# Kernel tuning notes

Hardware: AMD Instinct MI355X
Metric: run time of the kernel (lower is better)

Reference implementation:

```python
import jax, jax.numpy as jnp
import numpy as np

SITE, DIM = 8, 16
B = 8192
D = 2 * DIM

# --- static Z2-graded (Grassmann) bookkeeping -------------------------------
# Each edge (d, d) has parity 0 for the first d indices, parity 1 for the rest.
# Merging two graded edges reorders the flat product index so that all
# even-parity combinations come first (stable/lex within each sector).

def _merge_order(pA, pB):
    p = (pA[:, None] ^ pB[None, :]).reshape(-1)
    return np.argsort(p, kind='stable')

_P1 = np.array([0, 1])                                        # edge (1,1)
_PD = np.concatenate([np.zeros(DIM, np.int64), np.ones(DIM, np.int64)])  # edge (d,d)
ORDER_DD = _merge_order(_PD, _PD); INV_DD = np.argsort(ORDER_DD)
ORDER_1D = _merge_order(_P1, _PD); INV_1D = np.argsort(ORDER_1D)
ORDER_11 = _merge_order(_P1, _P1)                             # = [0,3,1,2]
MASK_X = jnp.asarray((_P1[:, None] ^ _PD[None, :]) == 0, jnp.float32)   # (2, D)
MASK_G2 = jnp.asarray((_PD[:, None] ^ _PD[None, :]) == 0, jnp.float32)  # (D, D)
MASK_G3 = jnp.asarray((_PD[:, None, None] ^ _PD[None, :, None] ^ _PD[None, None, :]) == 0, jnp.float32)
SIGN_PD = jnp.asarray(1.0 - 2.0 * _PD, jnp.float32)           # (-1)^parity, reverse sign
SWSIGN = jnp.asarray((-1.0) ** (_P1[:, None] * _PD[None, :]), jnp.float32)  # swap sign (2, D)


def setup_inputs() -> dict:
    key = jax.random.key(0)
    k1, k2, k3, k4 = jax.random.split(key, 4)
    return {
        'data': jax.random.randint(k1, (B, SITE), 0, 2),
        'embedding': jax.random.normal(k2, (SITE, 2, DIM), jnp.float32),
        'head_w': jax.random.normal(k3, (D, D), jnp.float32),
        'body_w': jax.random.normal(k4, (SITE - 1, D, D, D), jnp.float32),
    }


def _embed(emb_table, bits):
    # emb_table: (2, DIM); bits: (B,) in {0,1}
    emb = emb_table[bits]                                     # (B, DIM)
    zero = jnp.zeros_like(emb)
    on = bits[:, None] != 0
    row0 = jnp.concatenate([jnp.where(on, 0.0, emb), zero], -1)   # slot 0 (even,even)
    row1 = jnp.concatenate([zero, jnp.where(on, emb, 0.0)], -1)   # slot 3 (odd,odd)
    return jnp.stack([row0, row1], 1) * MASK_X                # (B, 2, D), even parity


def _body(x1, x2, g3):
    # x1, x2: (B, 2, D); g3: (D, D, D) with arrows (T, T, F)
    b = x1.shape[0]
    g = g3 * MASK_G3
    g = g * SIGN_PD[None, :, None]                            # reverse axis 1 (arrow flip)
    g_m = g.reshape(D, D * D)[:, ORDER_DD]                    # merge axes 1,2 even-first
    gx1 = jnp.einsum('bsk,km->bsm', x1 * MASK_X, g_m)         # (B, 2, D*D)
    gx1 = gx1[..., INV_DD].reshape(b, 2, D, D)                # split merged edge back
    gx1 = gx1 * SIGN_PD[None, None, :, None]                  # reverse axis 2
    gx1 = gx1 * SWSIGN[None, :, :, None]                      # graded sign: swap axes 1,2
    gx1_m = jnp.transpose(gx1, (0, 2, 1, 3)).reshape(b, D, 2 * D)[..., ORDER_1D]
    gx12 = jnp.einsum('bsk,bkm->bsm', x2 * MASK_X, gx1_m)     # (B, 2, 2D)
    gx12 = gx12[..., INV_1D].reshape(b, 2, 2, D)              # split into (s1 edge, (d,d))
    gx12 = gx12.reshape(b, 4, D)[:, ORDER_11, :]              # merge (s2, s1) even-first
    return gx12.reshape(b, 2, 2, D).sum(2)                    # sum per parity sector -> (B, 2, D)


def reference(data, embedding, head_w, body_w):
    x = _embed(embedding[0], data[:, 0])
    x = jnp.tanh(jnp.einsum('bsk,kj->bsj', x, head_w * MASK_G2))
    for i in range(1, SITE):
        x = jnp.tanh(_body(x, _embed(embedding[i], data[:, i]), body_w[i - 1]))
    return x
```

## Files before the change

kernel.cpp:

```cpp
#include <hip/hip_runtime.h>
#include <cmath>

#define SITE 8
#define DIM 16
#define BATCH 8192
#define NPAT 256

__global__ __launch_bounds__(256) void pattern_kernel(
    const float* __restrict__ embedding,
    const float* __restrict__ head_w,
    const float* __restrict__ body_w,
    float* __restrict__ pat)
{
    __shared__ float M[7][2][2][256];
    __shared__ float hv[2][16];
    __shared__ float st[8][2][16];

    const int tid = threadIdx.x;
    const int pbase = blockIdx.x * 8;

    {
        const int k = tid >> 4;
        const int j = tid & 15;
        for (int r = 0; r < 28; ++r) {
            int s   = r >> 2;
            int bit = (r >> 1) & 1;
            int h   = r & 1;
            const float* g3  = body_w + s * 32768;
            const float* emb = embedding + (s + 1) * 32 + bit * 16;
            float acc = 0.f;
            if (bit == 0) {
                if (h == 0) {
                    #pragma unroll
                    for (int i = 0; i < 16; ++i) acc += emb[i] * g3[k*1024 + i*32 + j];
                } else {
                    #pragma unroll
                    for (int i = 0; i < 16; ++i) acc += emb[i] * g3[(k+16)*1024 + i*32 + (j+16)];
                }
            } else {
                if (h == 0) {
                    #pragma unroll
                    for (int i = 0; i < 16; ++i) acc -= emb[i] * g3[(k+16)*1024 + (i+16)*32 + j];
                } else {
                    #pragma unroll
                    for (int i = 0; i < 16; ++i) acc += emb[i] * g3[k*1024 + (i+16)*32 + (j+16)];
                }
            }
            M[s][bit][h][tid & 255] = acc;
        }
    }

    if (tid < 32) {
        int h = tid >> 4;
        int j = tid & 15;
        const float* emb = embedding + h * 16;
        float a = 0.f;
        if (h == 0) {
            #pragma unroll
            for (int k = 0; k < 16; ++k) a += emb[k] * head_w[k*32 + j];
        } else {
            #pragma unroll
            for (int k = 0; k < 16; ++k) a += emb[k] * head_w[(k+16)*32 + (j+16)];
        }
        hv[h][j] = tanhf(a);
    }
    __syncthreads();

    {
        int pl = tid >> 5;
        int h  = (tid >> 4) & 1;
        int j  = tid & 15;
        int bit0 = (pbase + pl) & 1;
        st[pl][h][j] = (h == bit0) ? hv[h][j] : 0.f;
    }
    __syncthreads();

    for (int s = 1; s < SITE; ++s) {
        int pl = tid >> 5;
        int h  = (tid >> 4) & 1;
        int j  = tid & 15;
        int bit = ((pbase + pl) >> s) & 1;
        const float* src = st[pl][h ^ bit];
        const float* m   = &M[s-1][bit][h][0];
        float a = 0.f;
        #pragma unroll
        for (int k = 0; k < 16; ++k) a += src[k] * m[k*16 + j];
        float nv = tanhf(a);
        __syncthreads();
        st[pl][h][j] = nv;
        __syncthreads();
    }

    {
        int pl = tid >> 5;
        int h  = (tid >> 4) & 1;
        int j  = tid & 15;
        pat[(pbase + pl) * 32 + h * 16 + j] = st[pl][h][j];
    }
}

__global__ __launch_bounds__(256) void scatter_kernel(
    const int* __restrict__ data,
    const float4* __restrict__ pat4,
    float4* __restrict__ out4)
{
    int gid = blockIdx.x * 256 + threadIdx.x;
    int b = gid >> 4;
    int q = gid & 15;
    const int4* d4 = (const int4*)(data + b * 8);
    int4 w0 = d4[0];
    int4 w1 = d4[1];
    int id = (w0.x & 1) | ((w0.y & 1) << 1) | ((w0.z & 1) << 2) | ((w0.w & 1) << 3)
           | ((w1.x & 1) << 4) | ((w1.y & 1) << 5) | ((w1.z & 1) << 6) | ((w1.w & 1) << 7);
    float4 v = make_float4(0.f, 0.f, 0.f, 0.f);
    if (q < 4)       v = pat4[id * 8 + q];
    else if (q >= 12) v = pat4[id * 8 + (q - 8)];
    out4[b * 16 + q] = v;
}

extern "C" void kernel_launch(void* const* d_in, const int* in_sizes, int n_in,
                              void* d_out, int out_size, void* d_ws, size_t ws_size,
                              hipStream_t stream) {
    const int*   data      = (const int*)d_in[0];
    const float* embedding = (const float*)d_in[1];
    const float* head_w    = (const float*)d_in[2];
    const float* body_w    = (const float*)d_in[3];
    float* pat = (float*)d_ws;

    pattern_kernel<<<32, 256, 0, stream>>>(embedding, head_w, body_w, pat);
    scatter_kernel<<<(BATCH * 16) / 256, 256, 0, stream>>>(data, (const float4*)pat,
                                                           (float4*)d_out);
}
```

Baseline: 78.51 us.

## Fuse pattern table and scatter into one kernel computing rows directly

```diff
diff --git a/kernel.cpp b/kernel.cpp
--- a/kernel.cpp
+++ b/kernel.cpp
@@ -4,20 +4,19 @@
 #define SITE 8
 #define DIM 16
 #define BATCH 8192
-#define NPAT 256
 
-__global__ __launch_bounds__(256) void pattern_kernel(
+__global__ __launch_bounds__(256) void fused_kernel(
+    const int* __restrict__ data,
     const float* __restrict__ embedding,
     const float* __restrict__ head_w,
     const float* __restrict__ body_w,
-    float* __restrict__ pat)
+    float* __restrict__ out)
 {
     __shared__ float M[7][2][2][256];
     __shared__ float hv[2][16];
-    __shared__ float st[8][2][16];
+    __shared__ __align__(16) float st[8][2][16];
 
     const int tid = threadIdx.x;
-    const int pbase = blockIdx.x * 8;
 
     {
         const int k = tid >> 4;
@@ -46,7 +45,7 @@
                     for (int i = 0; i < 16; ++i) acc += emb[i] * g3[k*1024 + (i+16)*32 + (j+16)];
                 }
             }
-            M[s][bit][h][tid & 255] = acc;
+            M[s][bit][h][tid] = acc;
         }
     }
 
@@ -66,56 +65,42 @@
     }
     __syncthreads();
 
-    {
-        int pl = tid >> 5;
-        int h  = (tid >> 4) & 1;
-        int j  = tid & 15;
-        int bit0 = (pbase + pl) & 1;
-        st[pl][h][j] = (h == bit0) ? hv[h][j] : 0.f;
+    const int pl = tid >> 5;
+    const int h  = (tid >> 4) & 1;
+    const int j  = tid & 15;
+    const int lane16 = tid & 15;
+
+    for (int rnd = 0; rnd < 8; ++rnd) {
+        const int b = blockIdx.x * 64 + rnd * 8 + pl;
+        const int4* d4 = (const int4*)(data + b * 8);
+        int4 w0 = d4[0];
+        int4 w1 = d4[1];
+        int id = (w0.x & 1) | ((w0.y & 1) << 1) | ((w0.z & 1) << 2) | ((w0.w & 1) << 3)
+               | ((w1.x & 1) << 4) | ((w1.y & 1) << 5) | ((w1.z & 1) << 6) | ((w1.w & 1) << 7);
+
+        float v = ((id & 1) == h) ? hv[h][j] : 0.f;
+        st[pl][h][j] = v;
+
+        #pragma unroll
+        for (int s = 1; s < SITE; ++s) {
+            int bit = (id >> s) & 1;
+            const float* src = st[pl][h ^ bit];
+            const float* m   = &M[s-1][bit][h][0];
+            float a = 0.f;
+            #pragma unroll
+            for (int k = 0; k < 16; ++k) a += src[k] * m[k*16 + j];
+            v = tanhf(a);
+            st[pl][h][j] = v;
+        }
+
+        if ((tid & 31) < 16) {
+            int q = lane16;
+            float4 v4 = make_float4(0.f, 0.f, 0.f, 0.f);
+            if (q < 4)        v4 = *(const float4*)&st[pl][0][q * 4];
+            else if (q >= 12) v4 = *(const float4*)&st[pl][1][(q - 12) * 4];
+            ((float4*)out)[b * 16 + q] = v4;
+        }
     }
-    __syncthreads();
-
-    for (int s = 1; s < SITE; ++s) {
-        int pl = tid >> 5;
-        int h  = (tid >> 4) & 1;
-        int j  = tid & 15;
-        int bit = ((pbase + pl) >> s) & 1;
-        const float* src = st[pl][h ^ bit];
-        const float* m   = &M[s-1][bit][h][0];
-        float a = 0.f;
-        #pragma unroll
-        for (int k = 0; k < 16; ++k) a += src[k] * m[k*16 + j];
-        float nv = tanhf(a);
-        __syncthreads();
-        st[pl][h][j] = nv;
-        __syncthreads();
-    }
-
-    {
-        int pl = tid >> 5;
-        int h  = (tid >> 4) & 1;
-        int j  = tid & 15;
-        pat[(pbase + pl) * 32 + h * 16 + j] = st[pl][h][j];
-    }
-}
-
-__global__ __launch_bounds__(256) void scatter_kernel(
-    const int* __restrict__ data,
-    const float4* __restrict__ pat4,
-    float4* __restrict__ out4)
-{
-    int gid = blockIdx.x * 256 + threadIdx.x;
-    int b = gid >> 4;
-    int q = gid & 15;
-    const int4* d4 = (const int4*)(data + b * 8);
-    int4 w0 = d4[0];
-    int4 w1 = d4[1];
-    int id = (w0.x & 1) | ((w0.y & 1) << 1) | ((w0.z & 1) << 2) | ((w0.w & 1) << 3)
-           | ((w1.x & 1) << 4) | ((w1.y & 1) << 5) | ((w1.z & 1) << 6) | ((w1.w & 1) << 7);
-    float4 v = make_float4(0.f, 0.f, 0.f, 0.f);
-    if (q < 4)       v = pat4[id * 8 + q];
-    else if (q >= 12) v = pat4[id * 8 + (q - 8)];
-    out4[b * 16 + q] = v;
 }
 
 extern "C" void kernel_launch(void* const* d_in, const int* in_sizes, int n_in,
@@ -125,9 +110,8 @@
     const float* embedding = (const float*)d_in[1];
     const float* head_w    = (const float*)d_in[2];
     const float* body_w    = (const float*)d_in[3];
-    float* pat = (float*)d_ws;
+    (void)d_ws; (void)ws_size;
 
-    pattern_kernel<<<32, 256, 0, stream>>>(embedding, head_w, body_w, pat);
-    scatter_kernel<<<(BATCH * 16) / 256, 256, 0, stream>>>(data, (const float4*)pat,
-                                                           (float4*)d_out);
+    fused_kernel<<<128, 256, 0, stream>>>(data, embedding, head_w, body_w,
+                                          (float*)d_out);
 }
```

Result: slower. 91.62 us (+16.7%).
